# Performance work log

Measured on AMD Instinct MI355X. Metric: run time of the kernel, lower is better.

## Reference

```python
import jax, jax.numpy as jnp
import numpy as np

N = 50000
IN_CH = 128
HID = 32
HEADS = 4
OUT_CH = 64
NEG_SLOPE = 0.2


def glorot(key, shape):
    fan = shape[0] + shape[-1] if len(shape) > 1 else shape[0]
    s = jnp.sqrt(6.0 / fan)
    return jax.random.uniform(key, shape, jnp.float32, -s, s)


def setup_inputs() -> dict:
    key = jax.random.key(0)
    ks = jax.random.split(key, 10)
    x = jax.random.normal(ks[0], (N, IN_CH), jnp.float32)
    edge_index = jax.random.randint(ks[1], (2, 800000), 0, N, jnp.int32)
    return {
        "x": x,
        "edge_index": edge_index,
        # layer 1 (heads=4, concat)
        "W1": glorot(ks[2], (IN_CH, HEADS * HID)),
        "att_src1": glorot(ks[3], (HEADS, HID)),
        "att_dst1": glorot(ks[4], (HEADS, HID)),
        "b1": jnp.zeros((HEADS * HID,), jnp.float32),
        # layer 2 (heads=1, no concat)
        "W2": glorot(ks[5], (HEADS * HID, OUT_CH)),
        "att_src2": glorot(ks[6], (1, OUT_CH)),
        "att_dst2": glorot(ks[7], (1, OUT_CH)),
        "b2": jnp.zeros((OUT_CH,), jnp.float32),
    }


def gat_conv(x, src, dst, W, att_src, att_dst, b, heads, out_ch, concat):
    n = x.shape[0]
    h = (x @ W).reshape(n, heads, out_ch)                  # [N,H,C]
    a_s = jnp.einsum("nhc,hc->nh", h, att_src)            # [N,H]
    a_d = jnp.einsum("nhc,hc->nh", h, att_dst)            # [N,H]
    e = jax.nn.leaky_relu(a_s[src] + a_d[dst], NEG_SLOPE)  # [E,H]
    # segment softmax over incoming edges of each destination node
    m = jax.ops.segment_max(e, dst, num_segments=n)
    ex = jnp.exp(e - m[dst])
    denom = jax.ops.segment_sum(ex, dst, num_segments=n)
    alpha = ex / (denom[dst] + 1e-16)                      # [E,H]
    msg = h[src] * alpha[:, :, None]                       # [E,H,C]
    out = jax.ops.segment_sum(msg, dst, num_segments=n)    # [N,H,C]
    out = out.reshape(n, heads * out_ch) if concat else out.mean(axis=1)
    return out + b


def _forward(x, edge_index, W1, att_src1, att_dst1, b1, W2, att_src2, att_dst2, b2):
    n = x.shape[0]
    loop = jnp.arange(n, dtype=edge_index.dtype)
    src = jnp.concatenate([edge_index[0], loop])  # PyG adds self-loops
    dst = jnp.concatenate([edge_index[1], loop])
    h = gat_conv(x, src, dst, W1, att_src1, att_dst1, b1, HEADS, HID, True)
    h = jax.nn.relu(h)
    return gat_conv(h, src, dst, W2, att_src2, att_dst2, b2, 1, OUT_CH, False)


def reference(x, edge_index, W1, att_src1, att_dst1, b1, W2, att_src2, att_dst2, b2):
    return _forward(x, edge_index, W1, att_src1, att_dst1, b1, W2, att_src2, att_dst2, b2)
```

## Files before the change

### kernel.cpp

```cpp
#include <hip/hip_runtime.h>

#define NEG_SLOPE 0.2f

typedef unsigned int uint32;
typedef unsigned short ushort;
typedef unsigned long long u64;
typedef __fp16 f16x2 __attribute__((ext_vector_type(2)));
typedef __fp16 half8 __attribute__((ext_vector_type(8)));
typedef float f32x4 __attribute__((ext_vector_type(4)));

constexpr int IN_CH = 128;
constexpr int HID = 32;
constexpr int HEADS = 4;
constexpr int OUT_CH = 64;
constexpr int C1 = HEADS * HID;
constexpr int RB = 1024;

__device__ inline uint32 pk_f16(float lo, float hi) {
    f16x2 h = __builtin_amdgcn_cvt_pkrtz(lo, hi);
    uint32 r;
    __builtin_memcpy(&r, &h, 4);
    return r;
}
__device__ inline float f16_lo(uint32 v) {
    f16x2 h;
    __builtin_memcpy(&h, &v, 4);
    return (float)h[0];
}
__device__ inline float f16_hi(uint32 v) {
    f16x2 h;
    __builtin_memcpy(&h, &v, 4);
    return (float)h[1];
}
__device__ inline float leaky(float e) {
    return fmaxf(e, 0.f) + NEG_SLOPE * fminf(e, 0.f);
}


__global__ __launch_bounds__(256) void pack_hist_kernel(const int* __restrict__ ei, int E,
                                                        uint32* __restrict__ packed,
                                                        int* __restrict__ ghist, int nblocks) {
    __shared__ int lh[256];
    int t = threadIdx.x;
    lh[t] = 0;
    __syncthreads();
    int base0 = blockIdx.x * RB;
#pragma unroll
    for (int j = 0; j < 4; j++) {
        int e = base0 + j * 256 + t;
        if (e < E) {
            uint32 s = (uint32)ei[e], d = (uint32)ei[E + e];
            uint32 v = (d << 16) | s;
            packed[e] = v;
            atomicAdd(&lh[v >> 24], 1);
        }
    }
    __syncthreads();
    ghist[(size_t)t * nblocks + blockIdx.x] = lh[t];
}

__global__ __launch_bounds__(256) void gscanA_kernel(int* __restrict__ a, int* __restrict__ bsums,
                                                     int L) {
    __shared__ int tsum[256];
    int t = threadIdx.x;
    int base = blockIdx.x * 2048 + t * 8;
    int v[8];
    int s = 0;
#pragma unroll
    for (int i = 0; i < 8; i++) {
        v[i] = (base + i < L) ? a[base + i] : 0;
        s += v[i];
    }
    tsum[t] = s;
    __syncthreads();
    for (int d = 1; d < 256; d <<= 1) {
        int x = (t >= d) ? tsum[t - d] : 0;
        __syncthreads();
        tsum[t] += x;
        __syncthreads();
    }
    int ex = (t > 0) ? tsum[t - 1] : 0;
    if (t == 255) bsums[blockIdx.x] = tsum[255];
#pragma unroll
    for (int i = 0; i < 8; i++) {
        if (base + i < L) a[base + i] = ex;
        ex += v[i];
    }
}

__global__ void gscanB_kernel(int* __restrict__ bsums, int nb) {
    int lane = threadIdx.x;
    int v0 = (lane < nb) ? bsums[lane] : 0;
    int v1 = (64 + lane < nb) ? bsums[64 + lane] : 0;
    int s0 = v0;
#pragma unroll
    for (int d = 1; d < 64; d <<= 1) {
        int o = __shfl_up(s0, d);
        if (lane >= d) s0 += o;
    }
    int tot0 = __shfl(s0, 63);
    int s1 = v1;
#pragma unroll
    for (int d = 1; d < 64; d <<= 1) {
        int o = __shfl_up(s1, d);
        if (lane >= d) s1 += o;
    }
    s1 += tot0;
    if (lane < nb) bsums[lane] = s0 - v0;
    if (64 + lane < nb) bsums[64 + lane] = s1 - v1;
}

__global__ void gscanC_kernel(int* __restrict__ a, const int* __restrict__ bsums, int L) {
    int i = blockIdx.x * blockDim.x + threadIdx.x;
    if (i < L) a[i] += bsums[i / 2048];
}

__global__ __launch_bounds__(256) void scatter_msd_kernel(const uint32* __restrict__ in,
                                                          uint32* __restrict__ out,
                                                          const int* __restrict__ gbase, int E,
                                                          int nblocks) {
    __shared__ int lbase[256];
    int t = threadIdx.x;
    lbase[t] = gbase[(size_t)t * nblocks + blockIdx.x];
    __syncthreads();
    int base0 = blockIdx.x * RB;
#pragma unroll
    for (int j = 0; j < 4; j++) {
        int e = base0 + j * 256 + t;
        if (e < E) {
            uint32 v = in[e];
            int slot = atomicAdd(&lbase[v >> 24], 1);
            out[slot] = v;
        }
    }
}

__global__ __launch_bounds__(256) void local_sort_kernel(const uint32* __restrict__ in,
                                                         uint32* __restrict__ out,
                                                         const int* __restrict__ ghist, int nblocks,
                                                         int* __restrict__ offsets, int N, int E) {
    __shared__ int hist[256];
    __shared__ int cum[256];
    int b = blockIdx.x;
    int t = threadIdx.x;
    int segstart = ghist[(size_t)b * nblocks];
    int segend = (b + 1 < 256) ? ghist[(size_t)(b + 1) * nblocks] : E;
    hist[t] = 0;
    __syncthreads();
    for (int i = segstart + t; i < segend; i += 256) atomicAdd(&hist[(in[i] >> 16) & 0xff], 1);
    __syncthreads();
    int v = hist[t];
    cum[t] = v;
    __syncthreads();
    for (int d = 1; d < 256; d <<= 1) {
        int x = (t >= d) ? cum[t - d] : 0;
        __syncthreads();
        cum[t] += x;
        __syncthreads();
    }
    int myExcl = cum[t] - v;
    int dstv = b * 256 + t;
    if (dstv < N) offsets[dstv] = segstart + myExcl;
    if (b == 0 && t == 0) offsets[N] = E;
    hist[t] = myExcl;
    __syncthreads();
    for (int i = segstart + t; i < segend; i += 256) {
        uint32 w = in[i];
        int slot = atomicAdd(&hist[(w >> 16) & 0xff], 1);
        out[segstart + slot] = w;
    }
}


template <int K, int COLS, int H, bool AF16>
__global__ __launch_bounds__(256) void gemm_dots_kernel(
    const float* __restrict__ A, const float* __restrict__ W,
    const float* __restrict__ att_s, const float* __restrict__ att_d,
    uint32* __restrict__ hb, float* __restrict__ as_, float* __restrict__ ad_, int N) {
    static_assert(K == 128, "");
    constexpr int CF = COLS / 16;
    __shared__ ushort xs[64][136];
    __shared__ ushort wt[COLS][136];
    int tid = threadIdx.x;
    int row0 = blockIdx.x * 64;

#pragma unroll
    for (int l = 0; l < 4; l++) {
        int idx = tid + l * 256;
        int row = idx >> 4, kc = idx & 15;
        uint4 pkv = make_uint4(0, 0, 0, 0);
        if (row0 + row < N) {
            if constexpr (AF16) {
                pkv = *(const uint4*)((const uint32*)A + (size_t)(row0 + row) * (K / 2) + kc * 4);
            } else {
                const float* ap = A + (size_t)(row0 + row) * K + kc * 8;
                float4 v0 = *(const float4*)ap;
                float4 v1 = *(const float4*)(ap + 4);
                pkv = make_uint4(pk_f16(v0.x, v0.y), pk_f16(v0.z, v0.w), pk_f16(v1.x, v1.y),
                                 pk_f16(v1.z, v1.w));
            }
        }
        *(uint4*)&xs[row][kc * 8] = pkv;
    }
    constexpr int NP = (K / 2) * COLS / 256;
#pragma unroll
    for (int l = 0; l < NP; l++) {
        int p = tid + l * 256;
        int col = p % COLS, kp = p / COLS;
        float v0 = W[(size_t)(2 * kp) * COLS + col];
        float v1 = W[(size_t)(2 * kp + 1) * COLS + col];
        *(uint32*)&wt[col][kp * 2] = pk_f16(v0, v1);
    }
    __syncthreads();

    int w = tid >> 6, l = tid & 63;
    int q = l & 15, g = l >> 4;

    half8 af[4];
#pragma unroll
    for (int ks = 0; ks < 4; ks++) af[ks] = *(const half8*)&xs[w * 16 + q][ks * 32 + g * 8];

    f32x4 accs[CF];
#pragma unroll
    for (int cf = 0; cf < CF; cf++) {
        f32x4 a = {0.f, 0.f, 0.f, 0.f};
#pragma unroll
        for (int ks = 0; ks < 4; ks++) {
            half8 bf = *(const half8*)&wt[cf * 16 + q][ks * 32 + g * 8];
            a = __builtin_amdgcn_mfma_f32_16x16x32_f16(af[ks], bf, a, 0, 0, 0);
        }
        accs[cf] = a;
    }

    float asf[CF], adf[CF];
#pragma unroll
    for (int cf = 0; cf < CF; cf++) {
        asf[cf] = att_s[cf * 16 + q];
        adf[cf] = att_d[cf * 16 + q];
    }

#pragma unroll
    for (int r = 0; r < 4; r++) {
        int n_r = row0 + w * 16 + g * 4 + r;
        uint32 dw[CF];
        float p0 = 0.f, p1 = 0.f, p2 = 0.f, p3 = 0.f;
        float d0 = 0.f, d1 = 0.f, d2 = 0.f, d3 = 0.f;
#pragma unroll
        for (int cf = 0; cf < CF; cf++) {
            float v = accs[cf][r];
            float nb = __shfl_xor(v, 1);
            float ev = (q & 1) ? nb : v;
            float ov = (q & 1) ? v : nb;
            dw[cf] = pk_f16(ev, ov);
            float cs = v * asf[cf], cd = v * adf[cf];
            if constexpr (H == 4) {
                if (cf < 2) {
                    p0 += cs;
                    d0 += cd;
                } else if (cf < 4) {
                    p1 += cs;
                    d1 += cd;
                } else if (cf < 6) {
                    p2 += cs;
                    d2 += cd;
                } else {
                    p3 += cs;
                    d3 += cd;
                }
            } else {
                p0 += cs;
                d0 += cd;
            }
        }
#pragma unroll
        for (int dd = 1; dd < 16; dd <<= 1) {
            p0 += __shfl_xor(p0, dd);
            d0 += __shfl_xor(d0, dd);
            if constexpr (H == 4) {
                p1 += __shfl_xor(p1, dd);
                d1 += __shfl_xor(d1, dd);
                p2 += __shfl_xor(p2, dd);
                d2 += __shfl_xor(d2, dd);
                p3 += __shfl_xor(p3, dd);
                d3 += __shfl_xor(d3, dd);
            }
        }
        if (n_r < N) {
            if ((q & 1) == 0) {
                uint32* hp = hb + (size_t)n_r * (COLS / 2) + (q >> 1);
#pragma unroll
                for (int cf = 0; cf < CF; cf++) hp[cf * 8] = dw[cf];
            }
            if constexpr (H == 4) {
                if ((q >> 2) == r) {
                    int hh = q & 3;
                    float vs = hh == 0 ? p0 : hh == 1 ? p1 : hh == 2 ? p2 : p3;
                    float vd = hh == 0 ? d0 : hh == 1 ? d1 : hh == 2 ? d2 : d3;
                    as_[(size_t)n_r * 4 + hh] = vs;
                    ad_[(size_t)n_r * 4 + hh] = vd;
                }
            } else {
                if (q == r) {
                    as_[n_r] = p0;
                    ad_[n_r] = d0;
                }
            }
        }
    }
}


template <int C, int H, bool RELU, bool OUTF16>
__global__ __launch_bounds__(256) void aggregate_kernel(
    const uint32* __restrict__ hb, const float* __restrict__ as_,
    const float* __restrict__ ad_, const int* __restrict__ offsets,
    const uint32* __restrict__ csr, const float* __restrict__ bias, void* __restrict__ outp,
    int N) {
    __shared__ float plds[4][64 * H];
    __shared__ int slds[4][64];
    int gid = blockIdx.x * blockDim.x + threadIdx.x;
    int n = gid >> 6;
    int lane = threadIdx.x & 63;
    int wslot = threadIdx.x >> 6;
    if (n >= N) return;
    int off = offsets[n];
    int deg = offsets[n + 1] - off;

    float ad[H], s[H];
#pragma unroll
    for (int h = 0; h < H; h++) {
        ad[h] = ad_[(size_t)n * H + h];
        s[h] = 0.f;
    }

    constexpr int G = C / 8;
    constexpr int EPI = 64 / G;
    int eg = lane / G;
    int cl = lane % G;
    int hsel = (H == 4) ? (cl >> 2) : 0;
    float acc[8];
#pragma unroll
    for (int j = 0; j < 8; j++) acc[j] = 0.f;

    for (int base = 0; base <= deg; base += 64) {
        int my = base + lane;
        int cnt = min(64, deg + 1 - base);
        if (my <= deg) {
            int si = (my < deg) ? (int)(csr[off + my] & 0xffffu) : n;
            slds[wslot][lane] = si;
            if constexpr (H == 4) {
                float4 a = ((const float4*)as_)[si];
                float q0 = __expf(fminf(leaky(a.x + ad[0]), 80.f));
                float q1 = __expf(fminf(leaky(a.y + ad[1]), 80.f));
                float q2 = __expf(fminf(leaky(a.z + ad[2]), 80.f));
                float q3 = __expf(fminf(leaky(a.w + ad[3]), 80.f));
                s[0] += q0;
                s[1] += q1;
                s[2] += q2;
                s[3] += q3;
                ((float4*)plds[wslot])[lane] = make_float4(q0, q1, q2, q3);
            } else {
                float p = __expf(fminf(leaky(as_[si] + ad[0]), 80.f));
                s[0] += p;
                plds[wslot][lane] = p;
            }
        }
        int t2 = 0;
        for (; t2 + 2 * EPI <= cnt; t2 += 2 * EPI) {
            int tA = t2 + eg, tB = t2 + EPI + eg;
            int srcA = slds[wslot][tA];
            int srcB = slds[wslot][tB];
            float alA = plds[wslot][tA * H + hsel];
            float alB = plds[wslot][tB * H + hsel];
            uint4 uA = *(const uint4*)(hb + (size_t)srcA * (C / 2) + cl * 4);
            uint4 uB = *(const uint4*)(hb + (size_t)srcB * (C / 2) + cl * 4);
            acc[0] = fmaf(alA, f16_lo(uA.x), acc[0]);
            acc[1] = fmaf(alA, f16_hi(uA.x), acc[1]);
            acc[2] = fmaf(alA, f16_lo(uA.y), acc[2]);
            acc[3] = fmaf(alA, f16_hi(uA.y), acc[3]);
            acc[4] = fmaf(alA, f16_lo(uA.z), acc[4]);
            acc[5] = fmaf(alA, f16_hi(uA.z), acc[5]);
            acc[6] = fmaf(alA, f16_lo(uA.w), acc[6]);
            acc[7] = fmaf(alA, f16_hi(uA.w), acc[7]);
            acc[0] = fmaf(alB, f16_lo(uB.x), acc[0]);
            acc[1] = fmaf(alB, f16_hi(uB.x), acc[1]);
            acc[2] = fmaf(alB, f16_lo(uB.y), acc[2]);
            acc[3] = fmaf(alB, f16_hi(uB.y), acc[3]);
            acc[4] = fmaf(alB, f16_lo(uB.z), acc[4]);
            acc[5] = fmaf(alB, f16_hi(uB.z), acc[5]);
            acc[6] = fmaf(alB, f16_lo(uB.w), acc[6]);
            acc[7] = fmaf(alB, f16_hi(uB.w), acc[7]);
        }
        for (; t2 < cnt; t2 += EPI) {
            int te = t2 + eg;
            bool valid = te < cnt;
            int tc = valid ? te : 0;
            int src = slds[wslot][tc];
            float al = plds[wslot][tc * H + hsel];
            al = valid ? al : 0.f;
            uint4 u = *(const uint4*)(hb + (size_t)src * (C / 2) + cl * 4);
            acc[0] = fmaf(al, f16_lo(u.x), acc[0]);
            acc[1] = fmaf(al, f16_hi(u.x), acc[1]);
            acc[2] = fmaf(al, f16_lo(u.y), acc[2]);
            acc[3] = fmaf(al, f16_hi(u.y), acc[3]);
            acc[4] = fmaf(al, f16_lo(u.z), acc[4]);
            acc[5] = fmaf(al, f16_hi(u.z), acc[5]);
            acc[6] = fmaf(al, f16_lo(u.w), acc[6]);
            acc[7] = fmaf(al, f16_hi(u.w), acc[7]);
        }
    }

#pragma unroll
    for (int d = 1; d < 64; d <<= 1)
#pragma unroll
        for (int h = 0; h < H; h++) s[h] += __shfl_xor(s[h], d);
#pragma unroll
    for (int d = G; d < 64; d <<= 1)
#pragma unroll
        for (int j = 0; j < 8; j++) acc[j] += __shfl_xor(acc[j], d);

    if (eg == 0) {
        float inv = 1.f / s[hsel];
        int c = cl * 8;
        float o[8];
#pragma unroll
        for (int j = 0; j < 8; j++) {
            o[j] = fmaf(acc[j], inv, bias[c + j]);
            if (RELU) o[j] = fmaxf(o[j], 0.f);
        }
        if constexpr (OUTF16) {
            uint4 pkv = make_uint4(pk_f16(o[0], o[1]), pk_f16(o[2], o[3]), pk_f16(o[4], o[5]),
                                   pk_f16(o[6], o[7]));
            *(uint4*)((uint32*)outp + (size_t)n * (C / 2) + cl * 4) = pkv;
        } else {
            float* out = (float*)outp;
            *(float4*)(out + (size_t)n * C + c) = make_float4(o[0], o[1], o[2], o[3]);
            *(float4*)(out + (size_t)n * C + c + 4) = make_float4(o[4], o[5], o[6], o[7]);
        }
    }
}


extern "C" void kernel_launch(void* const* d_in, const int* in_sizes, int n_in,
                              void* d_out, int out_size, void* d_ws, size_t ws_size,
                              hipStream_t stream) {
    const float* x = (const float*)d_in[0];
    const int* ei = (const int*)d_in[1];
    const float* W1 = (const float*)d_in[2];
    const float* att_src1 = (const float*)d_in[3];
    const float* att_dst1 = (const float*)d_in[4];
    const float* b1 = (const float*)d_in[5];
    const float* W2 = (const float*)d_in[6];
    const float* att_src2 = (const float*)d_in[7];
    const float* att_dst2 = (const float*)d_in[8];
    const float* b2 = (const float*)d_in[9];

    int N = in_sizes[0] / IN_CH;
    int E = in_sizes[1] / 2;

    char* wsp = (char*)d_ws;
    size_t off = 0;
    auto carve = [&](size_t bytes) -> void* {
        void* p = wsp + off;
        off = (off + bytes + 255) & ~(size_t)255;
        return p;
    };
    int nblocks = (E + RB - 1) / RB;
    int L = 256 * nblocks;
    int nsb = (L + 2047) / 2048;

    uint32* packed = (uint32*)carve((size_t)E * 4);
    uint32* tmp = (uint32*)carve((size_t)E * 4);
    int* ghist = (int*)carve((size_t)L * 4);
    int* bsums = (int*)carve(4096);
    int* offsets = (int*)carve((size_t)(N + 1) * 4);
    uint32* h1b = (uint32*)carve((size_t)N * C1 * 2);
    uint32* h2b = (uint32*)carve((size_t)N * OUT_CH * 2);
    uint32* out1h = (uint32*)carve((size_t)N * C1 * 2);
    float* as1 = (float*)carve((size_t)N * HEADS * 4);
    float* ad1 = (float*)carve((size_t)N * HEADS * 4);
    float* as2 = (float*)carve((size_t)N * 4);
    float* ad2 = (float*)carve((size_t)N * 4);

    int nbuckets = (N + 255) / 256;
    pack_hist_kernel<<<nblocks, 256, 0, stream>>>(ei, E, packed, ghist, nblocks);
    gscanA_kernel<<<nsb, 256, 0, stream>>>(ghist, bsums, L);
    gscanB_kernel<<<1, 64, 0, stream>>>(bsums, nsb);
    gscanC_kernel<<<(L + 255) / 256, 256, 0, stream>>>(ghist, bsums, L);
    scatter_msd_kernel<<<nblocks, 256, 0, stream>>>(packed, tmp, ghist, E, nblocks);
    local_sort_kernel<<<nbuckets, 256, 0, stream>>>(tmp, packed, ghist, nblocks, offsets, N, E);

    int nwaveblocks = (N * 64 + 255) / 256;
    int ngemmblocks = (N + 63) / 64;

    gemm_dots_kernel<128, 128, 4, false>
        <<<ngemmblocks, 256, 0, stream>>>(x, W1, att_src1, att_dst1, h1b, as1, ad1, N);
    aggregate_kernel<128, 4, true, true>
        <<<nwaveblocks, 256, 0, stream>>>(h1b, as1, ad1, offsets, packed, b1, (void*)out1h, N);

    gemm_dots_kernel<128, 64, 1, true><<<ngemmblocks, 256, 0, stream>>>(
        (const float*)out1h, W2, att_src2, att_dst2, h2b, as2, ad2, N);
    aggregate_kernel<64, 1, false, false>
        <<<nwaveblocks, 256, 0, stream>>>(h2b, as2, ad2, offsets, packed, b2, d_out, N);
}
```

Baseline: 129.2 us.

## Replace per-block histogram scan with global atomic bucket counters in radix sort

```diff
diff --git a/kernel.cpp b/kernel.cpp
--- a/kernel.cpp
+++ b/kernel.cpp
@@ -39,7 +39,7 @@
 
 __global__ __launch_bounds__(256) void pack_hist_kernel(const int* __restrict__ ei, int E,
                                                         uint32* __restrict__ packed,
-                                                        int* __restrict__ ghist, int nblocks) {
+                                                        int* __restrict__ gcount) {
     __shared__ int lh[256];
     int t = threadIdx.x;
     lh[t] = 0;
@@ -56,95 +56,69 @@
         }
     }
     __syncthreads();
-    ghist[(size_t)t * nblocks + blockIdx.x] = lh[t];
-}
-
-__global__ __launch_bounds__(256) void gscanA_kernel(int* __restrict__ a, int* __restrict__ bsums,
-                                                     int L) {
-    __shared__ int tsum[256];
+    if (lh[t]) atomicAdd(&gcount[t], lh[t]);
+}
+
+__global__ __launch_bounds__(256) void bases_kernel(const int* __restrict__ gcount,
+                                                    int* __restrict__ gbase,
+                                                    int* __restrict__ cursor, int E) {
+    __shared__ int cum[256];
     int t = threadIdx.x;
-    int base = blockIdx.x * 2048 + t * 8;
-    int v[8];
-    int s = 0;
-#pragma unroll
-    for (int i = 0; i < 8; i++) {
-        v[i] = (base + i < L) ? a[base + i] : 0;
-        s += v[i];
-    }
-    tsum[t] = s;
+    int v = gcount[t];
+    cum[t] = v;
     __syncthreads();
     for (int d = 1; d < 256; d <<= 1) {
-        int x = (t >= d) ? tsum[t - d] : 0;
+        int x = (t >= d) ? cum[t - d] : 0;
         __syncthreads();
-        tsum[t] += x;
+        cum[t] += x;
         __syncthreads();
     }
-    int ex = (t > 0) ? tsum[t - 1] : 0;
-    if (t == 255) bsums[blockIdx.x] = tsum[255];
-#pragma unroll
-    for (int i = 0; i < 8; i++) {
-        if (base + i < L) a[base + i] = ex;
-        ex += v[i];
-    }
-}
-
-__global__ void gscanB_kernel(int* __restrict__ bsums, int nb) {
-    int lane = threadIdx.x;
-    int v0 = (lane < nb) ? bsums[lane] : 0;
-    int v1 = (64 + lane < nb) ? bsums[64 + lane] : 0;
-    int s0 = v0;
-#pragma unroll
-    for (int d = 1; d < 64; d <<= 1) {
-        int o = __shfl_up(s0, d);
-        if (lane >= d) s0 += o;
-    }
-    int tot0 = __shfl(s0, 63);
-    int s1 = v1;
-#pragma unroll
-    for (int d = 1; d < 64; d <<= 1) {
-        int o = __shfl_up(s1, d);
-        if (lane >= d) s1 += o;
-    }
-    s1 += tot0;
-    if (lane < nb) bsums[lane] = s0 - v0;
-    if (64 + lane < nb) bsums[64 + lane] = s1 - v1;
-}
-
-__global__ void gscanC_kernel(int* __restrict__ a, const int* __restrict__ bsums, int L) {
-    int i = blockIdx.x * blockDim.x + threadIdx.x;
-    if (i < L) a[i] += bsums[i / 2048];
+    int excl = cum[t] - v;
+    gbase[t] = excl;
+    cursor[t] = excl;
+    if (t == 255) gbase[256] = E;
 }
 
 __global__ __launch_bounds__(256) void scatter_msd_kernel(const uint32* __restrict__ in,
                                                           uint32* __restrict__ out,
-                                                          const int* __restrict__ gbase, int E,
-                                                          int nblocks) {
+                                                          int* __restrict__ cursor, int E) {
+    __shared__ int lcnt[256];
     __shared__ int lbase[256];
     int t = threadIdx.x;
-    lbase[t] = gbase[(size_t)t * nblocks + blockIdx.x];
+    lcnt[t] = 0;
     __syncthreads();
     int base0 = blockIdx.x * RB;
+    uint32 vals[4];
+    int bks[4], rank[4];
+    bool val[4];
 #pragma unroll
     for (int j = 0; j < 4; j++) {
         int e = base0 + j * 256 + t;
-        if (e < E) {
-            uint32 v = in[e];
-            int slot = atomicAdd(&lbase[v >> 24], 1);
-            out[slot] = v;
-        }
-    }
+        val[j] = e < E;
+        uint32 v = val[j] ? in[e] : 0u;
+        vals[j] = v;
+        int b = v >> 24;
+        bks[j] = b;
+        if (val[j]) rank[j] = atomicAdd(&lcnt[b], 1);
+    }
+    __syncthreads();
+    if (lcnt[t] > 0) lbase[t] = atomicAdd(&cursor[t], lcnt[t]);
+    __syncthreads();
+#pragma unroll
+    for (int j = 0; j < 4; j++)
+        if (val[j]) out[lbase[bks[j]] + rank[j]] = vals[j];
 }
 
 __global__ __launch_bounds__(256) void local_sort_kernel(const uint32* __restrict__ in,
                                                          uint32* __restrict__ out,
-                                                         const int* __restrict__ ghist, int nblocks,
+                                                         const int* __restrict__ gbase,
                                                          int* __restrict__ offsets, int N, int E) {
     __shared__ int hist[256];
     __shared__ int cum[256];
     int b = blockIdx.x;
     int t = threadIdx.x;
-    int segstart = ghist[(size_t)b * nblocks];
-    int segend = (b + 1 < 256) ? ghist[(size_t)(b + 1) * nblocks] : E;
+    int segstart = gbase[b];
+    int segend = gbase[b + 1];
     hist[t] = 0;
     __syncthreads();
     for (int i = segstart + t; i < segend; i += 256) atomicAdd(&hist[(in[i] >> 16) & 0xff], 1);
@@ -466,13 +440,12 @@
         return p;
     };
     int nblocks = (E + RB - 1) / RB;
-    int L = 256 * nblocks;
-    int nsb = (L + 2047) / 2048;
 
     uint32* packed = (uint32*)carve((size_t)E * 4);
     uint32* tmp = (uint32*)carve((size_t)E * 4);
-    int* ghist = (int*)carve((size_t)L * 4);
-    int* bsums = (int*)carve(4096);
+    int* gcount = (int*)carve(1024);
+    int* gbase = (int*)carve(1032);
+    int* cursor = (int*)carve(1024);
     int* offsets = (int*)carve((size_t)(N + 1) * 4);
     uint32* h1b = (uint32*)carve((size_t)N * C1 * 2);
     uint32* h2b = (uint32*)carve((size_t)N * OUT_CH * 2);
@@ -483,12 +456,11 @@
     float* ad2 = (float*)carve((size_t)N * 4);
 
     int nbuckets = (N + 255) / 256;
-    pack_hist_kernel<<<nblocks, 256, 0, stream>>>(ei, E, packed, ghist, nblocks);
-    gscanA_kernel<<<nsb, 256, 0, stream>>>(ghist, bsums, L);
-    gscanB_kernel<<<1, 64, 0, stream>>>(bsums, nsb);
-    gscanC_kernel<<<(L + 255) / 256, 256, 0, stream>>>(ghist, bsums, L);
-    scatter_msd_kernel<<<nblocks, 256, 0, stream>>>(packed, tmp, ghist, E, nblocks);
-    local_sort_kernel<<<nbuckets, 256, 0, stream>>>(tmp, packed, ghist, nblocks, offsets, N, E);
+    hipMemsetAsync(gcount, 0, 1024, stream);
+    pack_hist_kernel<<<nblocks, 256, 0, stream>>>(ei, E, packed, gcount);
+    bases_kernel<<<1, 256, 0, stream>>>(gcount, gbase, cursor, E);
+    scatter_msd_kernel<<<nblocks, 256, 0, stream>>>(packed, tmp, cursor, E);
+    local_sort_kernel<<<nbuckets, 256, 0, stream>>>(tmp, packed, gbase, offsets, N, E);
 
     int nwaveblocks = (N * 64 + 255) / 256;
     int ngemmblocks = (N + 63) / 64;
```

Result: slower. 153.4 us (+18.8%).
